# Kernel optimization log

Hardware: AMD Instinct MI355X
Metric: run time of the kernel (lower is better)

## Reference

```python
import jax, jax.numpy as jnp
import numpy as np

B, N, IN_DIM, D, P, C = 256, 2048, 2, 128, 2048, 10
LN_EPS = 1e-5
NORM_EPS = 1e-12


def setup_inputs() -> dict:
    key = jax.random.key(0)
    ks = jax.random.split(key, 9)
    X = jax.random.normal(ks[0], (B, N, IN_DIM), dtype=jnp.float32)
    # deterministic pair subsample (stands in for torch.combinations + randperm[:max_pairs])
    rng = np.random.default_rng(0)
    i = rng.integers(0, N, size=(P,))
    j = rng.integers(0, N, size=(P,))
    j = np.where(i == j, (j + 1) % N, j)  # i != j, as combinations(r=2) guarantees
    pairs = jnp.asarray(np.stack([np.minimum(i, j), np.maximum(i, j)], axis=1), dtype=jnp.int32)
    # proj: Linear(2, D) + LayerNorm(D) (+ ReLU)
    W1 = jax.random.normal(ks[1], (IN_DIM, D), dtype=jnp.float32) / jnp.sqrt(jnp.float32(IN_DIM))
    b1 = jnp.zeros((D,), jnp.float32)
    gamma = jnp.ones((D,), jnp.float32)
    beta = jnp.zeros((D,), jnp.float32)
    # mlp: Linear(D, D) -> ReLU -> Linear(D, C)
    Wm1 = jax.random.normal(ks[2], (D, D), dtype=jnp.float32) / jnp.sqrt(jnp.float32(D))
    bm1 = jnp.zeros((D,), jnp.float32)
    Wm2 = jax.random.normal(ks[3], (D, C), dtype=jnp.float32) / jnp.sqrt(jnp.float32(D))
    bm2 = jnp.zeros((C,), jnp.float32)
    # frozen sdi_memory: row-normalized gaussian [C, D]
    mem = jax.random.normal(ks[4], (C, D), dtype=jnp.float32)
    mem = mem / jnp.maximum(jnp.linalg.norm(mem, axis=1, keepdims=True), NORM_EPS)
    return {"X": X, "pairs": pairs, "W1": W1, "b1": b1, "gamma": gamma, "beta": beta,
            "Wm1": Wm1, "bm1": bm1, "Wm2": Wm2, "bm2": bm2, "mem": mem}


def reference(X, pairs, W1, b1, gamma, beta, Wm1, bm1, Wm2, bm2, mem):
    # proj: Linear + LayerNorm (biased var, like torch) + ReLU  -> z: [B, N, D]
    h = jnp.einsum('bni,id->bnd', X, W1) + b1
    mu = h.mean(-1, keepdims=True)
    var = ((h - mu) ** 2).mean(-1, keepdims=True)
    z = jax.nn.relu(gamma * (h - mu) * jax.lax.rsqrt(var + LN_EPS) + beta)
    # pairwise gather: diffs then sums, concatenated along pair axis -> [B, 2P, D]
    za = z[:, pairs[:, 0], :]
    zb = z[:, pairs[:, 1], :]
    feats = jnp.concatenate([za - zb, za + zb], axis=1)
    # row-wise L2 normalize (F.normalize, eps=1e-12), then mean over pairs -> sdi: [B, D]
    feats = feats / jnp.maximum(jnp.linalg.norm(feats, axis=-1, keepdims=True), NORM_EPS)
    sdi = feats.mean(axis=1)
    # logits = sdi @ mem.T + mlp(sdi)
    logits = sdi @ mem.T + (jax.nn.relu(sdi @ Wm1 + bm1) @ Wm2 + bm2)
    return logits, sdi
```

## Files before the change

kernel.cpp:

```cpp
#include <hip/hip_runtime.h>

#define B 256
#define N 2048
#define P 2048
#define C 10
#define S_CHUNKS 4
#define PPB (P / S_CHUNKS)
#define NIT (PPB / 32)
#define LN_EPS 1e-5f

typedef float v2f __attribute__((ext_vector_type(2)));
typedef _Float16 h2 __attribute__((ext_vector_type(2)));

static __device__ __forceinline__ float fdot2(h2 a, h2 b, float c) {
#if __has_builtin(__builtin_amdgcn_fdot2)
    return __builtin_amdgcn_fdot2(a, b, c, false);
#else
    return (float)a.x * (float)b.x + (float)a.y * (float)b.y + c;
#endif
}
static __device__ __forceinline__ h2 h2fma(h2 a, h2 b, h2 c) {
#if __has_builtin(__builtin_elementwise_fma)
    return __builtin_elementwise_fma(a, b, c);
#else
    return a * b + c;
#endif
}
static __device__ __forceinline__ h2 h2relu(h2 x) {
#if __has_builtin(__builtin_elementwise_max)
    return __builtin_elementwise_max(x, h2{(_Float16)0.f, (_Float16)0.f});
#else
    h2 r;
    r.x = x.x > (_Float16)0.f ? x.x : (_Float16)0.f;
    r.y = x.y > (_Float16)0.f ? x.y : (_Float16)0.f;
    return r;
#endif
}
static __device__ __forceinline__ h2 pkrtz(float a, float b) {
#if __has_builtin(__builtin_amdgcn_cvt_pkrtz)
    return __builtin_bit_cast(h2, __builtin_amdgcn_cvt_pkrtz(a, b));
#else
    return h2{(_Float16)a, (_Float16)b};
#endif
}
static __device__ __forceinline__ unsigned pk_rne(float a, float b) {
    return __builtin_bit_cast(unsigned, h2{(_Float16)a, (_Float16)b});
}

static __device__ __forceinline__ float red16(float x) {
    x += __int_as_float(__builtin_amdgcn_update_dpp(0, __float_as_int(x), 0xB1,  0xF, 0xF, true));
    x += __int_as_float(__builtin_amdgcn_update_dpp(0, __float_as_int(x), 0x4E,  0xF, 0xF, true));
    x += __int_as_float(__builtin_amdgcn_update_dpp(0, __float_as_int(x), 0x141, 0xF, 0xF, true));
    x += __int_as_float(__builtin_amdgcn_update_dpp(0, __float_as_int(x), 0x140, 0xF, 0xF, true));
    return x;
}

__global__ __launch_bounds__(256) void triple_kernel(
        const float* __restrict__ X,
        const float* __restrict__ W1, const float* __restrict__ b1,
        const float* __restrict__ gamma, const float* __restrict__ beta,
        unsigned* __restrict__ wsw, uint2* __restrict__ T) {
    const int t = threadIdx.x;
    __shared__ float r[6][128];
    __shared__ float sc[6];

    float w0 = 0.f, w1 = 0.f, bb = 0.f;
    if (t < 128) {
        w0 = W1[t]; w1 = W1[128 + t]; bb = b1[t];
        r[0][t] = w0; r[1][t] = w1; r[2][t] = bb;
    }
    __syncthreads();
    for (int s = 64; s > 0; s >>= 1) {
        if (t < s) { r[0][t] += r[0][t + s]; r[1][t] += r[1][t + s]; r[2][t] += r[2][t + s]; }
        __syncthreads();
    }
    const float m0 = r[0][0] * (1.f / 128.f);
    const float m1 = r[1][0] * (1.f / 128.f);
    const float mb = r[2][0] * (1.f / 128.f);
    __syncthreads();
    float c0 = 0.f, c1 = 0.f, cb = 0.f;
    if (t < 128) {
        c0 = w0 - m0; c1 = w1 - m1; cb = bb - mb;
        r[0][t] = c0 * c0; r[1][t] = c1 * c1; r[2][t] = cb * cb;
        r[3][t] = c0 * c1; r[4][t] = c0 * cb; r[5][t] = c1 * cb;
    }
    __syncthreads();
    for (int s = 64; s > 0; s >>= 1) {
        if (t < s) {
            #pragma unroll
            for (int q = 0; q < 6; ++q) r[q][t] += r[q][t + s];
        }
        __syncthreads();
    }
    if (t < 6) sc[t] = r[t][0] * (1.f / 128.f);
    __syncthreads();

    const float S00 = sc[0], S11 = sc[1], Sbb = sc[2];
    const float S01 = sc[3], S0b = sc[4], S1b = sc[5];

    if (t < 128) {
        const float g = gamma[t];
        r[0][t] = g * c0; r[1][t] = g * c1; r[2][t] = g * cb; r[3][t] = beta[t];
    }
    __syncthreads();
    if (blockIdx.x == 0 && t < 16) {
        uint4* dst = (uint4*)wsw + t * 4;
        #pragma unroll
        for (int m = 0; m < 4; ++m) {
            const int d0 = t + 32 * m, d1 = d0 + 16;
            dst[m] = uint4{pk_rne(r[0][d0], r[0][d1]), pk_rne(r[1][d0], r[1][d1]),
                           pk_rne(r[2][d0], r[2][d1]), pk_rne(r[3][d0], r[3][d1])};
        }
    }

    const int gid = blockIdx.x * 256 + t;
    const float2 x = ((const float2*)X)[gid];
    const float v = fmaf(x.x * x.x, S00, fmaf(x.y * x.y, S11, Sbb))
                  + 2.f * fmaf(x.x * x.y, S01, fmaf(x.x, S0b, x.y * S1b));
    const float rs = rsqrtf(v + LN_EPS);
    T[gid] = uint2{pk_rne(rs * x.x, rs * x.y), pk_rne(rs, 1.f)};
}

__global__ __launch_bounds__(256) void pair_kernel(
        const uint2*    __restrict__ T,
        const int*      __restrict__ pairs,
        const unsigned* __restrict__ wsw,
        float* __restrict__ part) {
    const int b = blockIdx.x;
    const int chunk = blockIdx.y;
    const int tid = threadIdx.x;
    const int w = tid >> 6, l = tid & 63, g = l >> 4, s = l & 15;
    const int slot = w * 4 + g;

    const uint4* Wl = (const uint4*)wsw + s * 4;
    h2 gw0[4], gw1[4], gbc[4], be2[4];
    #pragma unroll
    for (int m = 0; m < 4; ++m) {
        const uint4 wm = Wl[m];
        gw0[m] = __builtin_bit_cast(h2, wm.x);
        gw1[m] = __builtin_bit_cast(h2, wm.y);
        gbc[m] = __builtin_bit_cast(h2, wm.z);
        be2[m] = __builtin_bit_cast(h2, wm.w);
    }

    const uint2* Tb  = T + (size_t)b * N;
    const int4*  pr4 = (const int4*)pairs;
    const int i4base = chunk * (PPB / 2);

    v2f acc[4];
    #pragma unroll
    for (int m = 0; m < 4; ++m) acc[m] = v2f{0.f, 0.f};

    auto proc = [&](const uint2 ti, const uint2 tj) {
        const h2 abi = __builtin_bit_cast(h2, ti.x), ci = __builtin_bit_cast(h2, ti.y);
        const h2 abj = __builtin_bit_cast(h2, tj.x), cj = __builtin_bit_cast(h2, tj.y);
        const h2 aai = h2{abi.x, abi.x}, bbi = h2{abi.y, abi.y}, cci = h2{ci.x, ci.x};
        const h2 aaj = h2{abj.x, abj.x}, bbj = h2{abj.y, abj.y}, ccj = h2{cj.x, cj.x};
        h2 uu[4], vv[4];
        float nu = 0.f, nv = 0.f;
        #pragma unroll
        for (int m = 0; m < 4; ++m) {
            const h2 hi = h2relu(h2fma(aai, gw0[m], h2fma(bbi, gw1[m], h2fma(cci, gbc[m], be2[m]))));
            const h2 hj = h2relu(h2fma(aaj, gw0[m], h2fma(bbj, gw1[m], h2fma(ccj, gbc[m], be2[m]))));
            const h2 u = hi - hj;
            const h2 v = hi + hj;
            nu = fdot2(u, u, nu);
            nv = fdot2(v, v, nv);
            uu[m] = u; vv[m] = v;
        }
        nu = red16(nu);
        nv = red16(nv);
        const float ru = rsqrtf(fmaxf(nu, 1e-24f));
        const float rv = rsqrtf(fmaxf(nv, 1e-24f));
        const h2 ruv = pkrtz(ru, rv);
        #pragma unroll
        for (int m = 0; m < 4; ++m) {
            acc[m].x = fdot2(h2{uu[m].x, vv[m].x}, ruv, acc[m].x);
            acc[m].y = fdot2(h2{uu[m].y, vv[m].y}, ruv, acc[m].y);
        }
    };

    int4 idx = pr4[i4base + slot];
    uint2 tiA = Tb[idx.x], tjA = Tb[idx.y];

    for (int t = 0; t < NIT; ++t) {
        const uint2 tiB = Tb[idx.z], tjB = Tb[idx.w];
        int4 nidx = idx;
        if (t + 1 < NIT) nidx = pr4[i4base + (t + 1) * 16 + slot];

        proc(tiA, tjA);

        const uint2 ntiA = Tb[nidx.x], ntjA = Tb[nidx.y];

        proc(tiB, tjB);

        idx = nidx; tiA = ntiA; tjA = ntjA;
    }

    __shared__ float red[16][8][17];
    #pragma unroll
    for (int m = 0; m < 4; ++m) {
        red[slot][2 * m    ][s] = acc[m].x;
        red[slot][2 * m + 1][s] = acc[m].y;
    }
    __syncthreads();
    if (tid < 128) {
        const int ss = tid & 15, kk = tid >> 4;
        float sum = 0.f;
        #pragma unroll
        for (int q = 0; q < 16; ++q) sum += red[q][kk][ss];
        part[((size_t)b * S_CHUNKS + chunk) * 128 + tid] = sum;
    }
}

__global__ __launch_bounds__(256) void head_kernel(
        const float* __restrict__ part,
        const float* __restrict__ Wm1, const float* __restrict__ bm1,
        const float* __restrict__ Wm2, const float* __restrict__ bm2,
        const float* __restrict__ mem,
        float* __restrict__ out_logits, float* __restrict__ out_sdi) {
    const int b = blockIdx.x;
    const int t = threadIdx.x;
    __shared__ float s[128];
    __shared__ float h[128];

    if (t < 128) {
        float sv = 0.f;
        #pragma unroll
        for (int k = 0; k < S_CHUNKS; ++k)
            sv += part[((size_t)b * S_CHUNKS + k) * 128 + t];
        sv *= (1.f / (2.f * P));
        s[t] = sv;
        out_sdi[(size_t)b * 128 + t] = sv;
    }
    __syncthreads();
    if (t < 128) {
        float a = bm1[t];
        for (int d = 0; d < 128; ++d) a = fmaf(s[d], Wm1[d * 128 + t], a);
        h[t] = fmaxf(a, 0.f);
    }
    __syncthreads();
    if (t < 16 * C) {
        const int c = t >> 4, l = t & 15;
        float lg = 0.f;
        #pragma unroll
        for (int q = 0; q < 8; ++q) {
            const int d = l + 16 * q;
            lg = fmaf(s[d], mem[c * 128 + d], fmaf(h[d], Wm2[d * C + c], lg));
        }
        lg = red16(lg);
        if (l == 0) out_logits[(size_t)b * C + c] = lg + bm2[c];
    }
}

extern "C" void kernel_launch(void* const* d_in, const int* in_sizes, int n_in,
                              void* d_out, int out_size, void* d_ws, size_t ws_size,
                              hipStream_t stream) {
    const float* X     = (const float*)d_in[0];
    const int*   pairs = (const int*)  d_in[1];
    const float* W1    = (const float*)d_in[2];
    const float* b1    = (const float*)d_in[3];
    const float* gamma = (const float*)d_in[4];
    const float* beta  = (const float*)d_in[5];
    const float* Wm1   = (const float*)d_in[6];
    const float* bm1   = (const float*)d_in[7];
    const float* Wm2   = (const float*)d_in[8];
    const float* bm2   = (const float*)d_in[9];
    const float* mem   = (const float*)d_in[10];

    float* out = (float*)d_out;
    float* ws  = (float*)d_ws;
    unsigned* wsw  = (unsigned*)ws;
    uint2*    T    = (uint2*)(ws + 512);
    float*    part = ws + 512 + (size_t)B * N * 2;

    triple_kernel<<<(B * N) / 256, 256, 0, stream>>>(X, W1, b1, gamma, beta, wsw, T);
    pair_kernel<<<dim3(B, S_CHUNKS), 256, 0, stream>>>(T, pairs, wsw, part);
    head_kernel<<<B, 256, 0, stream>>>(part, Wm1, bm1, Wm2, bm2, mem,
                                       out, out + (size_t)B * C);
}
```

Baseline: 37.80 us.

## Stage per-batch T row in LDS and double pair chunks per batch

```diff
diff --git a/kernel.cpp b/kernel.cpp
--- a/kernel.cpp
+++ b/kernel.cpp
@@ -4,7 +4,7 @@
 #define N 2048
 #define P 2048
 #define C 10
-#define S_CHUNKS 4
+#define S_CHUNKS 8
 #define PPB (P / S_CHUNKS)
 #define NIT (PPB / 32)
 #define LN_EPS 1e-5f
@@ -132,6 +132,16 @@
     const int w = tid >> 6, l = tid & 63, g = l >> 4, s = l & 15;
     const int slot = w * 4 + g;
 
+    __shared__ __align__(16) float lds[4096];
+    uint2* Tl = (uint2*)lds;
+
+    {
+        const uint4* Tb4 = (const uint4*)(T + (size_t)b * N);
+        uint4* Tl4 = (uint4*)lds;
+        #pragma unroll
+        for (int q = 0; q < 4; ++q) Tl4[q * 256 + tid] = Tb4[q * 256 + tid];
+    }
+
     const uint4* Wl = (const uint4*)wsw + s * 4;
     h2 gw0[4], gw1[4], gbc[4], be2[4];
     #pragma unroll
@@ -143,9 +153,9 @@
         be2[m] = __builtin_bit_cast(h2, wm.w);
     }
 
-    const uint2* Tb  = T + (size_t)b * N;
-    const int4*  pr4 = (const int4*)pairs;
+    const int4* pr4 = (const int4*)pairs;
     const int i4base = chunk * (PPB / 2);
+    int4 idx = pr4[i4base + slot];
 
     v2f acc[4];
     #pragma unroll
@@ -157,19 +167,19 @@
         const h2 aai = h2{abi.x, abi.x}, bbi = h2{abi.y, abi.y}, cci = h2{ci.x, ci.x};
         const h2 aaj = h2{abj.x, abj.x}, bbj = h2{abj.y, abj.y}, ccj = h2{cj.x, cj.x};
         h2 uu[4], vv[4];
-        float nu = 0.f, nv = 0.f;
+        float nu0 = 0.f, nu1 = 0.f, nv0 = 0.f, nv1 = 0.f;
         #pragma unroll
         for (int m = 0; m < 4; ++m) {
             const h2 hi = h2relu(h2fma(aai, gw0[m], h2fma(bbi, gw1[m], h2fma(cci, gbc[m], be2[m]))));
             const h2 hj = h2relu(h2fma(aaj, gw0[m], h2fma(bbj, gw1[m], h2fma(ccj, gbc[m], be2[m]))));
             const h2 u = hi - hj;
             const h2 v = hi + hj;
-            nu = fdot2(u, u, nu);
-            nv = fdot2(v, v, nv);
+            if (m & 1) { nu1 = fdot2(u, u, nu1); nv1 = fdot2(v, v, nv1); }
+            else       { nu0 = fdot2(u, u, nu0); nv0 = fdot2(v, v, nv0); }
             uu[m] = u; vv[m] = v;
         }
-        nu = red16(nu);
-        nv = red16(nv);
+        const float nu = red16(nu0 + nu1);
+        const float nv = red16(nv0 + nv1);
         const float ru = rsqrtf(fmaxf(nu, 1e-24f));
         const float rv = rsqrtf(fmaxf(nv, 1e-24f));
         const h2 ruv = pkrtz(ru, rv);
@@ -180,35 +190,30 @@
         }
     };
 
-    int4 idx = pr4[i4base + slot];
-    uint2 tiA = Tb[idx.x], tjA = Tb[idx.y];
+    __syncthreads();
 
     for (int t = 0; t < NIT; ++t) {
-        const uint2 tiB = Tb[idx.z], tjB = Tb[idx.w];
-        int4 nidx = idx;
-        if (t + 1 < NIT) nidx = pr4[i4base + (t + 1) * 16 + slot];
-
+        const int4 nidx = (t + 1 < NIT) ? pr4[i4base + (t + 1) * 16 + slot] : idx;
+        const uint2 tiA = Tl[idx.x], tjA = Tl[idx.y];
+        const uint2 tiB = Tl[idx.z], tjB = Tl[idx.w];
         proc(tiA, tjA);
-
-        const uint2 ntiA = Tb[nidx.x], ntjA = Tb[nidx.y];
-
         proc(tiB, tjB);
-
-        idx = nidx; tiA = ntiA; tjA = ntjA;
-    }
-
-    __shared__ float red[16][8][17];
+        idx = nidx;
+    }
+
+    __syncthreads();
+
     #pragma unroll
     for (int m = 0; m < 4; ++m) {
-        red[slot][2 * m    ][s] = acc[m].x;
-        red[slot][2 * m + 1][s] = acc[m].y;
+        lds[slot * 136 + (2 * m)     * 17 + s] = acc[m].x;
+        lds[slot * 136 + (2 * m + 1) * 17 + s] = acc[m].y;
     }
     __syncthreads();
     if (tid < 128) {
         const int ss = tid & 15, kk = tid >> 4;
         float sum = 0.f;
         #pragma unroll
-        for (int q = 0; q < 16; ++q) sum += red[q][kk][ss];
+        for (int q = 0; q < 16; ++q) sum += lds[q * 136 + kk * 17 + ss];
         part[((size_t)b * S_CHUNKS + chunk) * 128 + tid] = sum;
     }
 }
```

Result: faster. 37.03 us (-2.0%).
